# Kernel tuning notes

Hardware: AMD Instinct MI355X
Metric: run time of the kernel (lower is better)

The kernel has to match this reference:

```python
import jax, jax.numpy as jnp
import numpy as np

N = 32768      # total nodes per batched graph
E = 262144     # edges per batched graph (avg in-degree 8)
B = 64         # number of graphs in the batch (for mean_nodes readout)
DIN = 20
H = 512
BN_EPS = 1e-5


def setup_inputs() -> dict:
    key = jax.random.key(0)
    ks = jax.random.split(key, 24)
    p = lambda k, shape: jax.random.normal(k, shape, jnp.float32) * 0.02
    inp = {
        "x1": jax.random.normal(ks[0], (N, DIN), jnp.float32),
        "x2": jax.random.normal(ks[1], (N, DIN), jnp.float32),
        "src1": jax.random.randint(ks[2], (E,), 0, N, jnp.int32),
        "dst1": jax.random.randint(ks[3], (E,), 0, N, jnp.int32),
        "src2": jax.random.randint(ks[4], (E,), 0, N, jnp.int32),
        "dst2": jax.random.randint(ks[5], (E,), 0, N, jnp.int32),
        "gids1": jnp.repeat(jnp.arange(B, dtype=jnp.int32), N // B),
        "gids2": jnp.repeat(jnp.arange(B, dtype=jnp.int32), N // B),
        # shared parameters (applied to both graphs, as in the torch module)
        "W_init": p(ks[6], (DIN, H)), "b_init": jnp.zeros((H,), jnp.float32),
        "W1": p(ks[7], (H, H)), "b1": jnp.zeros((H,), jnp.float32),
        "W2": p(ks[8], (H, H)), "b2": jnp.zeros((H,), jnp.float32),
        "gamma1": jnp.ones((H,), jnp.float32), "beta1": jnp.zeros((H,), jnp.float32),
        "gamma2": jnp.ones((H,), jnp.float32), "beta2": jnp.zeros((H,), jnp.float32),
        "Wfc": p(ks[9], (2 * H, 256)), "bfc": jnp.zeros((256,), jnp.float32),
        "Wfc2": p(ks[10], (256, 1)), "bfc2": jnp.zeros((1,), jnp.float32),
    }
    return inp


def _bn_relu(z, gamma, beta):
    # BatchNorm1d in training mode: biased batch stats over the node axis
    mu = jnp.mean(z, axis=0)
    var = jnp.var(z, axis=0)
    return jax.nn.relu(gamma * (z - mu) * jax.lax.rsqrt(var + BN_EPS) + beta)


def _gin_mean(h, src, dst, W, b):
    # DGL GINConv(apply=Linear, aggregator='mean', eps=0):
    # out = Linear(h + mean_{j in N_in(v)} h_j); isolated nodes get 0 agg.
    msg_sum = jax.ops.segment_sum(h[src], dst, num_segments=N)      # [N,H]
    deg = jax.ops.segment_sum(jnp.ones((src.shape[0],), h.dtype), dst, num_segments=N)
    agg = msg_sum / jnp.maximum(deg, 1.0)[:, None]
    return (h + agg) @ W + b


def _encode(x, src, dst, gids, W_init, b_init, W1, b1, W2, b2,
            gamma1, beta1, gamma2, beta2):
    h0 = x @ W_init + b_init
    h1 = _bn_relu(_gin_mean(h0, src, dst, W1, b1), gamma1, beta1)
    h2 = _bn_relu(_gin_mean(h1, src, dst, W2, b2), gamma2, beta2)
    # dgl.mean_nodes: per-graph mean over nodes
    s = jax.ops.segment_sum(h2, gids, num_segments=B)               # [B,H]
    cnt = jax.ops.segment_sum(jnp.ones((h2.shape[0],), h2.dtype), gids, num_segments=B)
    return s / jnp.maximum(cnt, 1.0)[:, None]


def reference(x1, x2, src1, dst1, src2, dst2, gids1, gids2,
              W_init, b_init, W1, b1, W2, b2,
              gamma1, beta1, gamma2, beta2, Wfc, bfc, Wfc2, bfc2):
    g1_emb = _encode(x1, src1, dst1, gids1, W_init, b_init, W1, b1, W2, b2,
                     gamma1, beta1, gamma2, beta2)
    g2_emb = _encode(x2, src2, dst2, gids2, W_init, b_init, W1, b1, W2, b2,
                     gamma1, beta1, gamma2, beta2)
    x = jnp.concatenate([g1_emb, g2_emb], axis=1)                   # [B,2H]
    x = jax.nn.relu(x @ Wfc + bfc)
    return jax.nn.sigmoid(x @ Wfc2 + bfc2)                          # [B,1]
```

## Files before the change

### kernel.cpp

```cpp
#include <hip/hip_runtime.h>
#include <hip/hip_bf16.h>
#include <cstdint>

#define NN 32768
#define EE 262144
#define MM 65536
#define HH 512
#define BB 64
#define DIN 20
#define BN_EPS 1e-5f

__device__ __forceinline__ float bflo(uint32_t w) { return __builtin_bit_cast(float, w << 16); }
__device__ __forceinline__ float bfhi(uint32_t w) { return __builtin_bit_cast(float, w & 0xffff0000u); }
__device__ __forceinline__ uint32_t f2bf_u(float f) {
  uint32_t u = __builtin_bit_cast(uint32_t, f);
  return (u + 0x7fffu + ((u >> 16) & 1u)) >> 16;
}
__device__ __forceinline__ uint32_t pack2(float lo, float hi) {
  return f2bf_u(lo) | (f2bf_u(hi) << 16);
}

typedef __bf16 bf16x8 __attribute__((ext_vector_type(8)));
typedef float f32x4 __attribute__((ext_vector_type(4)));
typedef float f32x2 __attribute__((ext_vector_type(2)));

__device__ __forceinline__ void gl2lds16(const void* g, void* l) {
  __builtin_amdgcn_global_load_lds(
      (const __attribute__((address_space(1))) void*)g,
      (__attribute__((address_space(3))) void*)l, 16, 0, 0);
}

__global__ void prep_deg_kernel(const int* __restrict__ dst1, const int* __restrict__ dst2,
                                int* __restrict__ deg_cnt,
                                const float* __restrict__ W2, uint16_t* __restrict__ Wt2,
                                const float* __restrict__ Wi, const float* __restrict__ bi,
                                const float* __restrict__ W1, float* __restrict__ Wf) {
  int bid = blockIdx.x;
  if (bid < 2048) {
    int e = bid * 256 + threadIdx.x;
    int g = e >> 18, le = e & 0x3ffff;
    int d = (g ? dst2 : dst1)[le];
    atomicAdd(&deg_cnt[g * NN + d], 1);
  } else if (bid < 2048 + 1024) {
    int i = (bid - 2048) * 256 + threadIdx.x;
    int n = i >> 9, k = i & 511;
    Wt2[i] = (uint16_t)f2bf_u(W2[(size_t)k * HH + n]);
  } else {
    int idx = (bid - 3072) * 256 + threadIdx.x;
    if (idx >= 21 * 512) return;
    int k = idx >> 9, n = idx & 511;
    float s = 0.f;
    if (k < 20) {
      const float* wr = Wi + (size_t)k * HH;
      for (int j = 0; j < HH; j++) s = fmaf(wr[j], W1[(size_t)j * HH + n], s);
    } else {
      for (int j = 0; j < HH; j++) s = fmaf(bi[j], W1[(size_t)j * HH + n], s);
    }
    Wf[idx] = s;
  }
}

__global__ void scan_kernel(const int* __restrict__ deg_cnt, int* __restrict__ offsets,
                            int* __restrict__ cursor) {
  int g = blockIdx.x;
  const int* d = deg_cnt + g * NN;
  int* off = offsets + g * (NN + 1);
  int* cur = cursor + g * NN;
  int t = threadIdx.x;
  int base = t * 32;
  int loc[32]; int s = 0;
#pragma unroll
  for (int i = 0; i < 32; i++) { loc[i] = d[base + i]; s += loc[i]; }
  __shared__ int sm[1024];
  sm[t] = s; __syncthreads();
  for (int ofs = 1; ofs < 1024; ofs <<= 1) {
    int v = sm[t];
    int add = (t >= ofs) ? sm[t - ofs] : 0;
    __syncthreads();
    sm[t] = v + add;
    __syncthreads();
  }
  int run = (t == 0) ? 0 : sm[t - 1];
#pragma unroll
  for (int i = 0; i < 32; i++) { off[base + i] = run; cur[base + i] = run; run += loc[i]; }
  if (t == 1023) off[NN] = run;
}

__global__ void scatter_kernel(const int* __restrict__ src1, const int* __restrict__ dst1,
                               const int* __restrict__ src2, const int* __restrict__ dst2,
                               int* __restrict__ cursor, int* __restrict__ csr) {
  int e = blockIdx.x * 256 + threadIdx.x;
  int g = e >> 18, le = e & 0x3ffff;
  int d = (g ? dst2 : dst1)[le];
  int s = (g ? src2 : src1)[le];
  int pos = atomicAdd(&cursor[g * NN + d], 1);
  csr[g * EE + pos] = s;
}

__global__ __launch_bounds__(256) void z1_kernel(const float* __restrict__ x1,
                          const float* __restrict__ x2,
                          const int* __restrict__ csr, const int* __restrict__ offsets,
                          const float* __restrict__ Wf, const float* __restrict__ b1,
                          uint16_t* __restrict__ z, uint32_t* __restrict__ z8,
                          float* __restrict__ pstat) {
  __shared__ float xas[128][21];
  int t = threadIdx.x;
  int r0 = blockIdx.x * 128;
  int g = r0 >> 15;
  const float* xg = g ? x2 : x1;
  const int* off = offsets + g * (NN + 1);
  const int* cs = csr + g * EE;

  {
    int row = t & 127;
    int half = t >> 7;
    int n = (r0 + row) & (NN - 1);
    int e0 = off[n], e1 = off[n + 1];
    int nf4 = half ? 2 : 3;
    int base4 = half ? 3 : 0;
    float4 a4[3] = {};
    for (int e = e0; e < e1; e++) {
      const float4* xr = (const float4*)(xg + (size_t)cs[e] * DIN) + base4;
      for (int k = 0; k < nf4; k++) {
        float4 v = xr[k];
        a4[k].x += v.x; a4[k].y += v.y; a4[k].z += v.z; a4[k].w += v.w;
      }
    }
    float inv = (e1 > e0) ? 1.f / (float)(e1 - e0) : 0.f;
    const float4* xs = (const float4*)(xg + (size_t)n * DIN) + base4;
    for (int k = 0; k < nf4; k++) {
      float4 v = xs[k];
      int d0 = (base4 + k) * 4;
      xas[row][d0 + 0] = fmaf(a4[k].x, inv, v.x);
      xas[row][d0 + 1] = fmaf(a4[k].y, inv, v.y);
      xas[row][d0 + 2] = fmaf(a4[k].z, inv, v.z);
      xas[row][d0 + 3] = fmaf(a4[k].w, inv, v.w);
    }
  }
  __syncthreads();

  int col0 = (t & 127) * 4;
  int rhalf = t >> 7;

  float w[DIN][4];
#pragma unroll
  for (int k = 0; k < DIN; k++) {
    float4 wv = *(const float4*)(Wf + (size_t)k * HH + col0);
    w[k][0] = wv.x; w[k][1] = wv.y; w[k][2] = wv.z; w[k][3] = wv.w;
  }
  float4 bvv = *(const float4*)(Wf + (size_t)DIN * HH + col0);
  float4 b1v = *(const float4*)(b1 + col0);

  float s4[4] = {0.f, 0.f, 0.f, 0.f}, q4[4] = {0.f, 0.f, 0.f, 0.f};
  for (int rr = 0; rr < 64; rr++) {
    int row = rr * 2 + rhalf;
    int grow = r0 + row;
    int n = grow & (NN - 1);
    float bf = (off[n + 1] - off[n] > 0) ? 2.f : 1.f;
    float a0 = fmaf(bvv.x, bf, b1v.x), a1 = fmaf(bvv.y, bf, b1v.y);
    float a2 = fmaf(bvv.z, bf, b1v.z), a3 = fmaf(bvv.w, bf, b1v.w);
#pragma unroll
    for (int k = 0; k < DIN; k++) {
      float xv = xas[row][k];
      a0 = fmaf(xv, w[k][0], a0);
      a1 = fmaf(xv, w[k][1], a1);
      a2 = fmaf(xv, w[k][2], a2);
      a3 = fmaf(xv, w[k][3], a3);
    }
    s4[0] += a0; q4[0] = fmaf(a0, a0, q4[0]);
    s4[1] += a1; q4[1] = fmaf(a1, a1, q4[1]);
    s4[2] += a2; q4[2] = fmaf(a2, a2, q4[2]);
    s4[3] += a3; q4[3] = fmaf(a3, a3, q4[3]);
    uint2 o;
    o.x = pack2(a0, a1); o.y = pack2(a2, a3);
    *(uint2*)(z + (size_t)grow * HH + col0) = o;
    uint32_t p8 = __builtin_amdgcn_cvt_pk_fp8_f32(a0, a1, 0u, false);
    p8 = __builtin_amdgcn_cvt_pk_fp8_f32(a2, a3, p8, true);
    z8[(size_t)grow * 128 + (col0 >> 2)] = p8;
  }

  __shared__ float sred[256][8];
#pragma unroll
  for (int k = 0; k < 4; k++) { sred[t][k] = s4[k]; sred[t][4 + k] = q4[k]; }
  __syncthreads();
  if (t < 128) {
    float* p = pstat + (size_t)blockIdx.x * 1024 + (size_t)col0 * 2;
#pragma unroll
    for (int k = 0; k < 4; k++) {
      p[k * 2 + 0] = sred[t][k] + sred[t + 128][k];
      p[k * 2 + 1] = sred[t][4 + k] + sred[t + 128][4 + k];
    }
  }
}

__global__ void reduce_stats(const float* __restrict__ pstat, const float* __restrict__ gamma,
                             const float* __restrict__ beta, float* __restrict__ scsh) {
  int b = blockIdx.x;
  int g = b >> 4, cg = b & 15;
  int t = threadIdx.x;
  int c = cg * 32 + (t & 31);
  int s = t >> 5;
  const float2* p = (const float2*)pstat + ((size_t)(g * 256 + s * 32)) * 512 + c;
  float sum = 0.f, q = 0.f;
  for (int m = 0; m < 32; m++) { float2 v = p[(size_t)m * 512]; sum += v.x; q += v.y; }
  __shared__ float ls[8][64];
  ls[s][(t & 31) * 2] = sum; ls[s][(t & 31) * 2 + 1] = q;
  __syncthreads();
  if (t < 32) {
    float S = 0.f, Q = 0.f;
#pragma unroll
    for (int k = 0; k < 8; k++) { S += ls[k][t * 2]; Q += ls[k][t * 2 + 1]; }
    int cc = cg * 32 + t;
    float mu = S * (1.f / (float)NN);
    float var = fmaxf(Q * (1.f / (float)NN) - mu * mu, 0.f);
    float sc = gamma[cc] * rsqrtf(var + BN_EPS);
    scsh[g * 1024 + cc * 2] = sc;
    scsh[g * 1024 + cc * 2 + 1] = beta[cc] - mu * sc;
  }
}

__device__ __forceinline__ void bn_acc8_fp8(uint2 v, const float* sc, const float* sh, float* acc) {
  f32x2 f01 = __builtin_amdgcn_cvt_pk_f32_fp8(v.x, false);
  f32x2 f23 = __builtin_amdgcn_cvt_pk_f32_fp8(v.x, true);
  f32x2 f45 = __builtin_amdgcn_cvt_pk_f32_fp8(v.y, false);
  f32x2 f67 = __builtin_amdgcn_cvt_pk_f32_fp8(v.y, true);
  acc[0] += fmaxf(fmaf(f01.x, sc[0], sh[0]), 0.f);
  acc[1] += fmaxf(fmaf(f01.y, sc[1], sh[1]), 0.f);
  acc[2] += fmaxf(fmaf(f23.x, sc[2], sh[2]), 0.f);
  acc[3] += fmaxf(fmaf(f23.y, sc[3], sh[3]), 0.f);
  acc[4] += fmaxf(fmaf(f45.x, sc[4], sh[4]), 0.f);
  acc[5] += fmaxf(fmaf(f45.y, sc[5], sh[5]), 0.f);
  acc[6] += fmaxf(fmaf(f67.x, sc[6], sh[6]), 0.f);
  acc[7] += fmaxf(fmaf(f67.y, sc[7], sh[7]), 0.f);
}

__global__ __launch_bounds__(256) void aggbn_kernel(const uint16_t* __restrict__ z,
                             const uint32_t* __restrict__ z8,
                             uint16_t* __restrict__ u,
                             const int* __restrict__ csr, const int* __restrict__ offsets,
                             const float* __restrict__ scsh) {
  int wid = (blockIdx.x * 256 + threadIdx.x) >> 6;
  int lane = threadIdx.x & 63;
  int g = wid >> 15, n = wid & (NN - 1);
  const int* off = offsets + g * (NN + 1);
  int e0 = off[n], e1 = off[n + 1];
  const int* cs = csr + g * EE;
  const uint32_t* hb = (const uint32_t*)z;
  const uint32_t* base = hb + (size_t)g * NN * 256 + lane * 4;
  const uint32_t* base8 = z8 + (size_t)g * NN * 128 + lane * 2;

  uint4 hv = *(const uint4*)(base + (size_t)n * 256);

  const float4* ssp = (const float4*)(scsh + (size_t)g * HH * 2 + lane * 16);
  float4 ss0 = ssp[0], ss1 = ssp[1], ss2 = ssp[2], ss3 = ssp[3];
  float sc[8] = {ss0.x, ss0.z, ss1.x, ss1.z, ss2.x, ss2.z, ss3.x, ss3.z};
  float sh[8] = {ss0.y, ss0.w, ss1.y, ss1.w, ss2.y, ss2.w, ss3.y, ss3.w};
  float acc[8] = {0.f, 0.f, 0.f, 0.f, 0.f, 0.f, 0.f, 0.f};

  int e = e0;
  int rem = e1 - e0;
  int s0 = 0, s1 = 0, s2 = 0, s3 = 0;
  if (rem >= 4) { s0 = cs[e]; s1 = cs[e + 1]; s2 = cs[e + 2]; s3 = cs[e + 3]; }
  while (rem >= 4) {
    uint2 v0 = *(const uint2*)(base8 + (size_t)s0 * 128);
    uint2 v1 = *(const uint2*)(base8 + (size_t)s1 * 128);
    uint2 v2 = *(const uint2*)(base8 + (size_t)s2 * 128);
    uint2 v3 = *(const uint2*)(base8 + (size_t)s3 * 128);
    e += 4; rem -= 4;
    if (rem >= 4) { s0 = cs[e]; s1 = cs[e + 1]; s2 = cs[e + 2]; s3 = cs[e + 3]; }
    bn_acc8_fp8(v0, sc, sh, acc);
    bn_acc8_fp8(v1, sc, sh, acc);
    bn_acc8_fp8(v2, sc, sh, acc);
    bn_acc8_fp8(v3, sc, sh, acc);
  }
  for (; rem > 0; rem--, e++) {
    int s = cs[e];
    uint2 v = *(const uint2*)(base8 + (size_t)s * 128);
    bn_acc8_fp8(v, sc, sh, acc);
  }

  float inv = (e1 > e0) ? 1.f / (float)(e1 - e0) : 0.f;
  uint32_t wv[4] = {hv.x, hv.y, hv.z, hv.w};
  float o[8];
#pragma unroll
  for (int i = 0; i < 4; i++) {
    o[2 * i]     = fmaxf(fmaf(bflo(wv[i]), sc[2 * i],     sh[2 * i]),     0.f) + acc[2 * i] * inv;
    o[2 * i + 1] = fmaxf(fmaf(bfhi(wv[i]), sc[2 * i + 1], sh[2 * i + 1]), 0.f) + acc[2 * i + 1] * inv;
  }
  uint4 ov;
  ov.x = pack2(o[0], o[1]); ov.y = pack2(o[2], o[3]); ov.z = pack2(o[4], o[5]); ov.w = pack2(o[6], o[7]);
  *(uint4*)((uint32_t*)u + (size_t)wid * 256 + lane * 4) = ov;
}

__global__ __launch_bounds__(256) void gemm_kernel(const uint16_t* __restrict__ A,
                                                   const uint16_t* __restrict__ Bt,
                                                   const float* __restrict__ bias,
                                                   uint16_t* __restrict__ C,
                                                   float* __restrict__ pstat) {
  __shared__ uint16_t sA[128 * 64];
  __shared__ uint16_t sB[128 * 64];
  const int tid = threadIdx.x;
  const int wave = tid >> 6;
  const int lane = tid & 63;
  const int bid = blockIdx.x;
  const int xcd = bid & 7;
  const int l = bid >> 3;
  const int nb = l & 3;
  const int mb = xcd * 64 + (l >> 2);
  const int m0 = mb * 128;
  const int n0 = nb * 128;
  const int fm = lane & 15;
  const int fm7 = fm & 7;
  const int quad = lane >> 4;
  const int wr = wave >> 1, wc = wave & 1;

  const int r_loc = lane >> 3;
  const int k8slot = lane & 7;
  const int k8g = k8slot ^ r_loc;
  const int rbase = wave * 32;

  f32x4 acc[4][4] = {};
  for (int k0 = 0; k0 < HH; k0 += 64) {
    __syncthreads();
#pragma unroll
    for (int t = 0; t < 4; t++) {
      int R = rbase + t * 8 + r_loc;
      gl2lds16(A  + (size_t)(m0 + R) * HH + k0 + k8g * 8, &sA[R * 64 + k8slot * 8]);
      gl2lds16(Bt + (size_t)(n0 + R) * HH + k0 + k8g * 8, &sB[R * 64 + k8slot * 8]);
    }
    __syncthreads();
#pragma unroll
    for (int s2 = 0; s2 < 2; s2++) {
      const int k8 = s2 * 4 + quad;
      bf16x8 a[4], b[4];
#pragma unroll
      for (int i = 0; i < 4; i++) {
        int r = wr * 64 + i * 16 + fm;
        a[i] = *(const bf16x8*)&sA[r * 64 + ((k8 ^ fm7) * 8)];
      }
#pragma unroll
      for (int j = 0; j < 4; j++) {
        int r = wc * 64 + j * 16 + fm;
        b[j] = *(const bf16x8*)&sB[r * 64 + ((k8 ^ fm7) * 8)];
      }
#pragma unroll
      for (int i = 0; i < 4; i++)
#pragma unroll
        for (int j = 0; j < 4; j++)
          acc[i][j] = __builtin_amdgcn_mfma_f32_16x16x32_bf16(a[i], b[j], acc[i][j], 0, 0, 0);
    }
  }
  __syncthreads();
  float* ls = (float*)sA;
  if (tid < 256) ls[tid] = 0.f;
  __syncthreads();
#pragma unroll
  for (int j = 0; j < 4; j++) {
    int colloc = wc * 64 + j * 16 + fm;
    int col = n0 + colloc;
    float bj = bias[col];
    float sj = 0.f, qj = 0.f;
#pragma unroll
    for (int i = 0; i < 4; i++) {
      int row = m0 + wr * 64 + i * 16 + quad * 4;
#pragma unroll
      for (int r = 0; r < 4; r++) {
        float f = acc[i][j][r] + bj;
        C[(size_t)(row + r) * HH + col] = (uint16_t)f2bf_u(f);
        sj += f; qj = fmaf(f, f, qj);
      }
    }
    atomicAdd(&ls[colloc * 2], sj);
    atomicAdd(&ls[colloc * 2 + 1], qj);
  }
  __syncthreads();
  if (tid < 128) {
    float* p = pstat + (size_t)mb * 1024 + (size_t)(n0 + tid) * 2;
    p[0] = ls[tid * 2];
    p[1] = ls[tid * 2 + 1];
  }
}

__global__ void bn2_readout(const uint16_t* __restrict__ z, const float* __restrict__ scsh,
                            const int* __restrict__ gids1, const int* __restrict__ gids2,
                            float* __restrict__ readout, float* __restrict__ cnt) {
  int blk = blockIdx.x;
  int r0 = blk * 128;
  int g = r0 >> 15;
  int lr = r0 & (NN - 1);
  int gid = (g ? gids2 : gids1)[lr];
  int t = threadIdx.x;
  int c = t * 2;
  const float* ss = scsh + (size_t)g * HH * 2;
  float sc0 = ss[c * 2], sh0 = ss[c * 2 + 1];
  float sc1 = ss[(c + 1) * 2], sh1 = ss[(c + 1) * 2 + 1];
  const uint32_t* p = (const uint32_t*)z + (size_t)r0 * 256 + t;
  float a0 = 0, a1 = 0;
  for (int r = 0; r < 128; r++) {
    uint32_t w = p[(size_t)r * 256];
    a0 += fmaxf(fmaf(bflo(w), sc0, sh0), 0.f);
    a1 += fmaxf(fmaf(bfhi(w), sc1, sh1), 0.f);
  }
  float* ro = readout + ((size_t)g * BB + gid) * HH;
  atomicAdd(&ro[c], a0);
  atomicAdd(&ro[c + 1], a1);
  if (t == 0) atomicAdd(&cnt[g * BB + gid], 128.f);
}

__global__ void final_kernel(const float* __restrict__ readout, const float* __restrict__ cnt,
                             const float* __restrict__ Wfc, const float* __restrict__ bfc,
                             const float* __restrict__ Wfc2, const float* __restrict__ bfc2,
                             float* __restrict__ out) {
  __shared__ float x[1024];
  __shared__ float red[256];
  int b = blockIdx.x, t = threadIdx.x;
  for (int i = t; i < 1024; i += 256) {
    int g = i >> 9, c = i & 511;
    float cc = cnt[g * BB + b];
    x[i] = readout[((size_t)g * BB + b) * HH + c] / fmaxf(cc, 1.f);
  }
  __syncthreads();
  float a0 = 0.f, a1 = 0.f, a2 = 0.f, a3 = 0.f;
  for (int i = 0; i < 1024; i += 4) {
    a0 = fmaf(x[i],     Wfc[(size_t)i * 256 + t],       a0);
    a1 = fmaf(x[i + 1], Wfc[(size_t)(i + 1) * 256 + t], a1);
    a2 = fmaf(x[i + 2], Wfc[(size_t)(i + 2) * 256 + t], a2);
    a3 = fmaf(x[i + 3], Wfc[(size_t)(i + 3) * 256 + t], a3);
  }
  float acc = bfc[t] + ((a0 + a1) + (a2 + a3));
  red[t] = fmaxf(acc, 0.f) * Wfc2[t];
  __syncthreads();
  for (int s = 128; s > 0; s >>= 1) {
    if (t < s) red[t] += red[t + s];
    __syncthreads();
  }
  if (t == 0) out[b] = 1.f / (1.f + expf(-(red[0] + bfc2[0])));
}

extern "C" void kernel_launch(void* const* d_in, const int* in_sizes, int n_in,
                              void* d_out, int out_size, void* d_ws, size_t ws_size,
                              hipStream_t stream) {
  const float* x1 = (const float*)d_in[0];
  const float* x2 = (const float*)d_in[1];
  const int* src1 = (const int*)d_in[2];
  const int* dst1 = (const int*)d_in[3];
  const int* src2 = (const int*)d_in[4];
  const int* dst2 = (const int*)d_in[5];
  const int* gids1 = (const int*)d_in[6];
  const int* gids2 = (const int*)d_in[7];
  const float* Wi = (const float*)d_in[8];
  const float* bi = (const float*)d_in[9];
  const float* W1 = (const float*)d_in[10];
  const float* b1 = (const float*)d_in[11];
  const float* W2 = (const float*)d_in[12];
  const float* b2 = (const float*)d_in[13];
  const float* gamma1 = (const float*)d_in[14];
  const float* beta1 = (const float*)d_in[15];
  const float* gamma2 = (const float*)d_in[16];
  const float* beta2 = (const float*)d_in[17];
  const float* Wfc = (const float*)d_in[18];
  const float* bfc = (const float*)d_in[19];
  const float* Wfc2 = (const float*)d_in[20];
  const float* bfc2 = (const float*)d_in[21];
  float* out = (float*)d_out;

  size_t off = 0;
  auto alloc = [&](size_t bytes) -> void* {
    void* p = (char*)d_ws + off;
    off += (bytes + 255) & ~(size_t)255;
    return p;
  };
  uint16_t* buf0 = (uint16_t*)alloc((size_t)MM * HH * 2);
  uint16_t* buf1 = (uint16_t*)alloc((size_t)MM * HH * 2);
  uint32_t* z8 = (uint32_t*)alloc((size_t)MM * HH);
  uint16_t* Wt2 = (uint16_t*)alloc((size_t)HH * HH * 2);
  float* Wf = (float*)alloc((size_t)(DIN + 1) * HH * 4);
  int* csr = (int*)alloc((size_t)2 * EE * 4);
  int* offsets = (int*)alloc((size_t)2 * (NN + 1) * 4);
  int* cursor = (int*)alloc((size_t)2 * NN * 4);
  float* pbuf1 = (float*)alloc((size_t)512 * 512 * 2 * 4);
  float* pbuf2 = (float*)alloc((size_t)512 * 512 * 2 * 4);
  size_t zero_begin = off;
  int* deg_cnt = (int*)alloc((size_t)2 * NN * 4);
  float* readout = (float*)alloc((size_t)2 * BB * HH * 4);
  float* cnt = (float*)alloc((size_t)2 * BB * 4);
  size_t zero_end = off;
  float* scsh1 = (float*)alloc((size_t)2 * HH * 2 * 4);
  float* scsh2 = (float*)alloc((size_t)2 * HH * 2 * 4);
  (void)ws_size; (void)in_sizes; (void)n_in; (void)out_size;

  hipMemsetAsync((char*)d_ws + zero_begin, 0, zero_end - zero_begin, stream);

  prep_deg_kernel<<<3072 + 42, 256, 0, stream>>>(dst1, dst2, deg_cnt, W2, Wt2, Wi, bi, W1, Wf);
  scan_kernel<<<2, 1024, 0, stream>>>(deg_cnt, offsets, cursor);
  scatter_kernel<<<2048, 256, 0, stream>>>(src1, dst1, src2, dst2, cursor, csr);

  z1_kernel<<<MM / 128, 256, 0, stream>>>(x1, x2, csr, offsets, Wf, b1, buf1, z8, pbuf1);
  reduce_stats<<<32, 256, 0, stream>>>(pbuf1, gamma1, beta1, scsh1);

  aggbn_kernel<<<MM / 4, 256, 0, stream>>>(buf1, z8, buf0, csr, offsets, scsh1);
  gemm_kernel<<<2048, 256, 0, stream>>>(buf0, Wt2, b2, buf1, pbuf2);
  reduce_stats<<<32, 256, 0, stream>>>(pbuf2, gamma2, beta2, scsh2);
  bn2_readout<<<MM / 128, 256, 0, stream>>>(buf1, scsh2, gids1, gids2, readout, cnt);

  final_kernel<<<BB, 256, 0, stream>>>(readout, cnt, Wfc, bfc, Wfc2, bfc2, out);
}
```

Baseline: 417.6 us.

## Run second GIN layer GEMM in FP8 with LDS-staged coalesced output stores

```diff
diff --git a/kernel.cpp b/kernel.cpp
--- a/kernel.cpp
+++ b/kernel.cpp
@@ -20,7 +20,6 @@
   return f2bf_u(lo) | (f2bf_u(hi) << 16);
 }
 
-typedef __bf16 bf16x8 __attribute__((ext_vector_type(8)));
 typedef float f32x4 __attribute__((ext_vector_type(4)));
 typedef float f32x2 __attribute__((ext_vector_type(2)));
 
@@ -32,7 +31,7 @@
 
 __global__ void prep_deg_kernel(const int* __restrict__ dst1, const int* __restrict__ dst2,
                                 int* __restrict__ deg_cnt,
-                                const float* __restrict__ W2, uint16_t* __restrict__ Wt2,
+                                const float* __restrict__ W2, uint32_t* __restrict__ Wt8,
                                 const float* __restrict__ Wi, const float* __restrict__ bi,
                                 const float* __restrict__ W1, float* __restrict__ Wf) {
   int bid = blockIdx.x;
@@ -41,12 +40,19 @@
     int g = e >> 18, le = e & 0x3ffff;
     int d = (g ? dst2 : dst1)[le];
     atomicAdd(&deg_cnt[g * NN + d], 1);
-  } else if (bid < 2048 + 1024) {
-    int i = (bid - 2048) * 256 + threadIdx.x;
-    int n = i >> 9, k = i & 511;
-    Wt2[i] = (uint16_t)f2bf_u(W2[(size_t)k * HH + n]);
+  } else if (bid < 2304) {
+    int idx = (bid - 2048) * 256 + threadIdx.x;
+    int n = idx >> 7, k4 = idx & 127;
+    int k = k4 * 4;
+    float w0 = W2[(size_t)k * HH + n];
+    float w1 = W2[(size_t)(k + 1) * HH + n];
+    float w2v = W2[(size_t)(k + 2) * HH + n];
+    float w3 = W2[(size_t)(k + 3) * HH + n];
+    uint32_t p = __builtin_amdgcn_cvt_pk_fp8_f32(w0, w1, 0u, false);
+    p = __builtin_amdgcn_cvt_pk_fp8_f32(w2v, w3, p, true);
+    Wt8[(size_t)n * 128 + k4] = p;
   } else {
-    int idx = (bid - 3072) * 256 + threadIdx.x;
+    int idx = (bid - 2304) * 256 + threadIdx.x;
     if (idx >= 21 * 512) return;
     int k = idx >> 9, n = idx & 511;
     float s = 0.f;
@@ -236,7 +242,7 @@
 
 __global__ __launch_bounds__(256) void aggbn_kernel(const uint16_t* __restrict__ z,
                              const uint32_t* __restrict__ z8,
-                             uint16_t* __restrict__ u,
+                             uint32_t* __restrict__ u8,
                              const int* __restrict__ csr, const int* __restrict__ offsets,
                              const float* __restrict__ scsh) {
   int wid = (blockIdx.x * 256 + threadIdx.x) >> 6;
@@ -287,18 +293,22 @@
     o[2 * i]     = fmaxf(fmaf(bflo(wv[i]), sc[2 * i],     sh[2 * i]),     0.f) + acc[2 * i] * inv;
     o[2 * i + 1] = fmaxf(fmaf(bfhi(wv[i]), sc[2 * i + 1], sh[2 * i + 1]), 0.f) + acc[2 * i + 1] * inv;
   }
-  uint4 ov;
-  ov.x = pack2(o[0], o[1]); ov.y = pack2(o[2], o[3]); ov.z = pack2(o[4], o[5]); ov.w = pack2(o[6], o[7]);
-  *(uint4*)((uint32_t*)u + (size_t)wid * 256 + lane * 4) = ov;
-}
-
-__global__ __launch_bounds__(256) void gemm_kernel(const uint16_t* __restrict__ A,
-                                                   const uint16_t* __restrict__ Bt,
+  uint32_t q0 = __builtin_amdgcn_cvt_pk_fp8_f32(o[0], o[1], 0u, false);
+  q0 = __builtin_amdgcn_cvt_pk_fp8_f32(o[2], o[3], q0, true);
+  uint32_t q1 = __builtin_amdgcn_cvt_pk_fp8_f32(o[4], o[5], 0u, false);
+  q1 = __builtin_amdgcn_cvt_pk_fp8_f32(o[6], o[7], q1, true);
+  uint2 ov; ov.x = q0; ov.y = q1;
+  *(uint2*)(u8 + (size_t)wid * 128 + lane * 2) = ov;
+}
+
+__global__ __launch_bounds__(256) void gemm_kernel(const uint8_t* __restrict__ A8,
+                                                   const uint8_t* __restrict__ Bt8,
                                                    const float* __restrict__ bias,
                                                    uint16_t* __restrict__ C,
                                                    float* __restrict__ pstat) {
-  __shared__ uint16_t sA[128 * 64];
-  __shared__ uint16_t sB[128 * 64];
+  __shared__ __align__(16) char lds[32768];
+  uint8_t* sA = (uint8_t*)lds;
+  uint8_t* sB = (uint8_t*)lds + 16384;
   const int tid = threadIdx.x;
   const int wave = tid >> 6;
   const int lane = tid & 63;
@@ -310,66 +320,66 @@
   const int m0 = mb * 128;
   const int n0 = nb * 128;
   const int fm = lane & 15;
-  const int fm7 = fm & 7;
   const int quad = lane >> 4;
   const int wr = wave >> 1, wc = wave & 1;
 
-  const int r_loc = lane >> 3;
-  const int k8slot = lane & 7;
-  const int k8g = k8slot ^ r_loc;
-  const int rbase = wave * 32;
+  const int sr = lane >> 3;
+  const int slot = lane & 7;
 
   f32x4 acc[4][4] = {};
-  for (int k0 = 0; k0 < HH; k0 += 64) {
+  for (int k0 = 0; k0 < HH; k0 += 128) {
     __syncthreads();
 #pragma unroll
     for (int t = 0; t < 4; t++) {
-      int R = rbase + t * 8 + r_loc;
-      gl2lds16(A  + (size_t)(m0 + R) * HH + k0 + k8g * 8, &sA[R * 64 + k8slot * 8]);
-      gl2lds16(Bt + (size_t)(n0 + R) * HH + k0 + k8g * 8, &sB[R * 64 + k8slot * 8]);
+      int R = t * 32 + wave * 8 + sr;
+      int ksw = (slot ^ (R & 7)) * 16;
+      gl2lds16(A8 + (size_t)(m0 + R) * HH + k0 + ksw, sA + R * 128 + slot * 16);
+      gl2lds16(Bt8 + (size_t)(n0 + R) * HH + k0 + ksw, sB + R * 128 + slot * 16);
     }
     __syncthreads();
 #pragma unroll
-    for (int s2 = 0; s2 < 2; s2++) {
+    for (int s2 = 0; s2 < 4; s2++) {
       const int k8 = s2 * 4 + quad;
-      bf16x8 a[4], b[4];
+      const int k16 = k8 >> 1;
+      const int h8 = (k8 & 1) * 8;
+      long a[4], b[4];
 #pragma unroll
       for (int i = 0; i < 4; i++) {
         int r = wr * 64 + i * 16 + fm;
-        a[i] = *(const bf16x8*)&sA[r * 64 + ((k8 ^ fm7) * 8)];
+        a[i] = *(const long*)(sA + r * 128 + ((k16 ^ (r & 7)) * 16) + h8);
       }
 #pragma unroll
       for (int j = 0; j < 4; j++) {
         int r = wc * 64 + j * 16 + fm;
-        b[j] = *(const bf16x8*)&sB[r * 64 + ((k8 ^ fm7) * 8)];
+        b[j] = *(const long*)(sB + r * 128 + ((k16 ^ (r & 7)) * 16) + h8);
       }
 #pragma unroll
       for (int i = 0; i < 4; i++)
 #pragma unroll
         for (int j = 0; j < 4; j++)
-          acc[i][j] = __builtin_amdgcn_mfma_f32_16x16x32_bf16(a[i], b[j], acc[i][j], 0, 0, 0);
-    }
-  }
-  __syncthreads();
-  float* ls = (float*)sA;
+          acc[i][j] = __builtin_amdgcn_mfma_f32_16x16x32_fp8_fp8(a[i], b[j], acc[i][j], 0, 0, 0);
+    }
+  }
+
+  float bj4[4];
+#pragma unroll
+  for (int j = 0; j < 4; j++) bj4[j] = bias[n0 + wc * 64 + j * 16 + fm];
+
+  __syncthreads();
+  float* ls = (float*)lds;
   if (tid < 256) ls[tid] = 0.f;
   __syncthreads();
 #pragma unroll
   for (int j = 0; j < 4; j++) {
     int colloc = wc * 64 + j * 16 + fm;
-    int col = n0 + colloc;
-    float bj = bias[col];
     float sj = 0.f, qj = 0.f;
 #pragma unroll
-    for (int i = 0; i < 4; i++) {
-      int row = m0 + wr * 64 + i * 16 + quad * 4;
+    for (int i = 0; i < 4; i++)
 #pragma unroll
       for (int r = 0; r < 4; r++) {
-        float f = acc[i][j][r] + bj;
-        C[(size_t)(row + r) * HH + col] = (uint16_t)f2bf_u(f);
+        float f = acc[i][j][r] + bj4[j];
         sj += f; qj = fmaf(f, f, qj);
       }
-    }
     atomicAdd(&ls[colloc * 2], sj);
     atomicAdd(&ls[colloc * 2 + 1], qj);
   }
@@ -378,6 +388,29 @@
     float* p = pstat + (size_t)mb * 1024 + (size_t)(n0 + tid) * 2;
     p[0] = ls[tid * 2];
     p[1] = ls[tid * 2 + 1];
+  }
+  __syncthreads();
+
+  uint16_t* sC = (uint16_t*)lds;
+#pragma unroll
+  for (int j = 0; j < 4; j++) {
+    int col = wc * 64 + j * 16 + fm;
+#pragma unroll
+    for (int i = 0; i < 4; i++) {
+      int rb = wr * 64 + i * 16 + quad * 4;
+#pragma unroll
+      for (int r = 0; r < 4; r++)
+        sC[(rb + r) * 128 + col] = (uint16_t)f2bf_u(acc[i][j][r] + bj4[j]);
+    }
+  }
+  __syncthreads();
+  const int orow = tid >> 4;
+  const int ocol = (tid & 15) * 8;
+#pragma unroll
+  for (int r8 = 0; r8 < 8; r8++) {
+    int row = r8 * 16 + orow;
+    uint4 v = *(const uint4*)(sC + row * 128 + ocol);
+    *(uint4*)(C + (size_t)(m0 + row) * HH + n0 + ocol) = v;
   }
 }
 
@@ -470,10 +503,10 @@
     off += (bytes + 255) & ~(size_t)255;
     return p;
   };
-  uint16_t* buf0 = (uint16_t*)alloc((size_t)MM * HH * 2);
   uint16_t* buf1 = (uint16_t*)alloc((size_t)MM * HH * 2);
   uint32_t* z8 = (uint32_t*)alloc((size_t)MM * HH);
-  uint16_t* Wt2 = (uint16_t*)alloc((size_t)HH * HH * 2);
+  uint32_t* u8 = (uint32_t*)alloc((size_t)MM * HH);
+  uint32_t* Wt8 = (uint32_t*)alloc((size_t)HH * HH);
   float* Wf = (float*)alloc((size_t)(DIN + 1) * HH * 4);
   int* csr = (int*)alloc((size_t)2 * EE * 4);
   int* offsets = (int*)alloc((size_t)2 * (NN + 1) * 4);
@@ -491,15 +524,15 @@
 
   hipMemsetAsync((char*)d_ws + zero_begin, 0, zero_end - zero_begin, stream);
 
-  prep_deg_kernel<<<3072 + 42, 256, 0, stream>>>(dst1, dst2, deg_cnt, W2, Wt2, Wi, bi, W1, Wf);
+  prep_deg_kernel<<<2304 + 42, 256, 0, stream>>>(dst1, dst2, deg_cnt, W2, Wt8, Wi, bi, W1, Wf);
   scan_kernel<<<2, 1024, 0, stream>>>(deg_cnt, offsets, cursor);
   scatter_kernel<<<2048, 256, 0, stream>>>(src1, dst1, src2, dst2, cursor, csr);
 
   z1_kernel<<<MM / 128, 256, 0, stream>>>(x1, x2, csr, offsets, Wf, b1, buf1, z8, pbuf1);
   reduce_stats<<<32, 256, 0, stream>>>(pbuf1, gamma1, beta1, scsh1);
 
-  aggbn_kernel<<<MM / 4, 256, 0, stream>>>(buf1, z8, buf0, csr, offsets, scsh1);
-  gemm_kernel<<<2048, 256, 0, stream>>>(buf0, Wt2, b2, buf1, pbuf2);
+  aggbn_kernel<<<MM / 4, 256, 0, stream>>>(buf1, z8, u8, csr, offsets, scsh1);
+  gemm_kernel<<<2048, 256, 0, stream>>>((const uint8_t*)u8, (const uint8_t*)Wt8, b2, buf1, pbuf2);
   reduce_stats<<<32, 256, 0, stream>>>(pbuf2, gamma2, beta2, scsh2);
   bn2_readout<<<MM / 128, 256, 0, stream>>>(buf1, scsh2, gids1, gids2, readout, cnt);
 
```

Measured after the change: 401.5 us. 3.9% less time.
